# Kernel tuning notes

Hardware: AMD Instinct MI355X
Metric: run time of the kernel (lower is better)

The kernel has to match this reference:

```python
import jax, jax.numpy as jnp
import numpy as np

E = 512        # emb_size
H = 2 * E      # LSTM units
B = 512        # beam/query batch (batched Python-loop states)
K = 32         # padded candidates per state
T = 8          # max_path_length
N_ENT = 50000
N_REL = 5000


def setup_inputs() -> dict:
    key = jax.random.key(0)
    ks = jax.random.split(key, 12)
    f32 = jnp.float32
    ent_emb = jax.random.normal(ks[0], (N_ENT, E), f32) * 0.05
    rel_emb = jax.random.normal(ks[1], (N_REL, E), f32) * 0.05
    relation = jax.random.normal(ks[2], (B, E), f32) * 0.05
    Wx = jax.random.normal(ks[3], (H, 4 * H), f32) * 0.02
    Wh = jax.random.normal(ks[4], (H, 4 * H), f32) * 0.02
    b = jnp.zeros((4 * H,), f32)
    W1 = jax.random.normal(ks[5], (4 * E, 3 * E), f32) * 0.02
    b1 = jnp.zeros((3 * E,), f32)
    W2 = jax.random.normal(ks[6], (3 * E, 2 * E), f32) * 0.02
    b2 = jnp.zeros((2 * E,), f32)
    current_ids = jax.random.randint(ks[7], (T, B), 0, N_ENT)
    prev_rel_ids = jax.random.randint(ks[8], (T, B), 0, N_REL)
    cand_rel_ids = jax.random.randint(ks[9], (T, B, K), 0, N_REL)
    cand_ent_ids = jax.random.randint(ks[10], (T, B, K), 0, N_ENT)
    return {
        "ent_emb": ent_emb, "rel_emb": rel_emb, "relation": relation,
        "Wx": Wx, "Wh": Wh, "b": b,
        "W1": W1, "b1": b1, "W2": W2, "b2": b2,
        "current_ids": current_ids, "prev_rel_ids": prev_rel_ids,
        "cand_rel_ids": cand_rel_ids, "cand_ent_ids": cand_ent_ids,
    }


def reference(ent_emb, rel_emb, relation, Wx, Wh, b, W1, b1, W2, b2,
              current_ids, prev_rel_ids, cand_rel_ids, cand_ent_ids):
    Bh = relation.shape[0]
    units = Wh.shape[0]
    h0 = jnp.zeros((Bh, units), ent_emb.dtype)
    c0 = jnp.zeros((Bh, units), ent_emb.dtype)

    def step(carry, xs):
        h, c = carry
        cur, prl, crel, cent = xs
        # LSTMCell input: concat(prev relation vec, current entity vec)  [B, 2E]
        x = jnp.concatenate([rel_emb[prl], ent_emb[cur]], axis=-1)
        z = x @ Wx + h @ Wh + b                      # [B, 4H], keras gate order i,f,g,o
        i_, f_, g_, o_ = jnp.split(z, 4, axis=-1)
        c = jax.nn.sigmoid(f_) * c + jax.nn.sigmoid(i_) * jnp.tanh(g_)
        h = jax.nn.sigmoid(o_) * jnp.tanh(c)
        # posterior MLP on concat(ent, history, relation)  [B, 4E] -> [B, 2E]
        feat = jax.nn.relu(jnp.concatenate([ent_emb[cur], h, relation], axis=-1) @ W1 + b1)
        feat = jax.nn.relu(feat @ W2 + b2)
        # candidate embeddings: concat(rel vec, to-entity vec)  [B, K, 2E]
        cand = jnp.concatenate([rel_emb[crel], ent_emb[cent]], axis=-1)
        probs = jax.nn.softmax(jnp.einsum('bkd,bd->bk', cand, feat), axis=-1)
        return (h, c), probs

    _, probs = jax.lax.scan(step, (h0, c0),
                            (current_ids, prev_rel_ids, cand_rel_ids, cand_ent_ids))
    return probs  # [T, B, K]
```

## Files before the change

kernel.cpp:

```cpp
#include <hip/hip_runtime.h>
#include <stdint.h>

typedef __attribute__((ext_vector_type(4))) float f32x4;
typedef __attribute__((ext_vector_type(8))) __bf16 bf16x8;
typedef __attribute__((ext_vector_type(8))) unsigned short u16x8;
typedef __attribute__((ext_vector_type(4))) unsigned short u16x4;

typedef const __attribute__((address_space(1))) unsigned int gu32;
typedef __attribute__((address_space(3))) unsigned int lu32;

__device__ __forceinline__ float b2f(unsigned short u) {
  unsigned int x = ((unsigned int)u) << 16;
  float f; __builtin_memcpy(&f, &x, 4); return f;
}
__device__ __forceinline__ unsigned short f2b(float f) {
  unsigned int x; __builtin_memcpy(&x, &f, 4);
  x += 0x7fffu + ((x >> 16) & 1u);
  return (unsigned short)(x >> 16);
}
__device__ __forceinline__ float sigmoidf(float x) {
  return 1.f / (1.f + __expf(-x));
}
__device__ __forceinline__ float tanh_fast(float x) {
  return 1.f - 2.f / (1.f + __expf(2.f * x));
}

__global__ __launch_bounds__(256) void prep1(
    const float* __restrict__ Wx, unsigned short* __restrict__ WxT,
    const float* __restrict__ Wh, unsigned short* __restrict__ WhT,
    const float* __restrict__ W1, unsigned short* __restrict__ W1T,
    const float* __restrict__ W2, unsigned short* __restrict__ W2T,
    const float* __restrict__ ent, const float* __restrict__ rel,
    const float* __restrict__ rln,
    const int* __restrict__ cur, const int* __restrict__ prl,
    unsigned short* __restrict__ Xall, unsigned short* __restrict__ ERall) {
  __shared__ unsigned short tile[64][72];
  const int tid = threadIdx.x;
  int b = blockIdx.x;
  if (b < 3200) {
    const float* in; unsigned short* out; int R, C, bx, by;
    if (b < 1024)      { in = Wx; out = WxT; R = 1024; C = 4096; bx = b & 63; by = b >> 6; }
    else if (b < 2048) { b -= 1024; in = Wh; out = WhT; R = 1024; C = 4096; bx = b & 63; by = b >> 6; }
    else if (b < 2816) { b -= 2048; in = W1; out = W1T; R = 2048; C = 1536; bx = b % 24; by = b / 24; }
    else               { b -= 2816; in = W2; out = W2T; R = 1536; C = 1024; bx = b & 15; by = b >> 4; }
    const int r0 = by * 64, c0 = bx * 64;
    const int r = tid >> 3;
    const int c8 = (tid & 7) * 8;
#pragma unroll
    for (int i = 0; i < 2; i++) {
      const int rr = r + 32*i;
      const float* src = in + (size_t)(r0 + rr) * C + c0 + c8;
      f32x4 a = *(const f32x4*)src;
      f32x4 bb = *(const f32x4*)(src + 4);
      unsigned short tmp[8];
#pragma unroll
      for (int j = 0; j < 4; j++) { tmp[j] = f2b(a[j]); tmp[4+j] = f2b(bb[j]); }
      *(u16x8*)(&tile[rr][c8 ^ (((rr >> 3) & 7) << 3)]) = *(u16x8*)tmp;
    }
    __syncthreads();
    const int rswz = (tid & 7) << 3;
#pragma unroll
    for (int i = 0; i < 2; i++) {
      const int ro = r + 32*i;
      unsigned short tmp[8];
#pragma unroll
      for (int j = 0; j < 8; j++) tmp[j] = tile[c8 + j][ro ^ rswz];
      *(u16x8*)(out + (size_t)(c0 + ro) * R + r0 + c8) = *(u16x8*)tmp;
    }
  } else {
    const int row = b - 3200;
    const int bb = row & 511;
    const int ci = cur[row], ri = prl[row];
    const int half = tid >> 7;
    const int j = tid & 127;
    const float* src;
    if (half == 0) src = (j < 64) ? (rel + (size_t)ri * 512 + j * 8)
                                  : (ent + (size_t)ci * 512 + (j - 64) * 8);
    else           src = (j < 64) ? (ent + (size_t)ci * 512 + j * 8)
                                  : (rln + (size_t)bb * 512 + (j - 64) * 8);
    f32x4 a = *(const f32x4*)src, c = *(const f32x4*)(src + 4);
    unsigned short t[8];
#pragma unroll
    for (int q = 0; q < 4; q++) { t[q] = f2b(a[q]); t[4+q] = f2b(c[q]); }
    unsigned short* dst = (half == 0 ? Xall : ERall) + (size_t)row * 1024 + j * 8;
    *(u16x8*)dst = *(u16x8*)t;
  }
}

__global__ __launch_bounds__(256) void conv_tables(
    const float* __restrict__ ent, unsigned short* __restrict__ entB,
    const float* __restrict__ rel, unsigned short* __restrict__ relB) {
  const long long N0 = 50000LL * 512 / 8, N1 = 5000LL * 512 / 8;
  long long i = (long long)blockIdx.x * 256 + threadIdx.x;
  if (i >= N0 + N1) return;
  const float* in; unsigned short* out;
  if (i < N0) { in = ent; out = entB; }
  else        { in = rel; out = relB; i -= N0; }
  f32x4 a = *(const f32x4*)(in + i * 8);
  f32x4 c = *(const f32x4*)(in + i * 8 + 4);
  unsigned short t[8];
#pragma unroll
  for (int q = 0; q < 4; q++) { t[q] = f2b(a[q]); t[4+q] = f2b(c[q]); }
  *(u16x8*)(out + i * 8) = *(u16x8*)t;
}

template<bool HAS_BIAS, bool DO_RELU, bool PERM_B, bool ASPLIT, bool LSTM0>
__global__ __launch_bounds__(256) void gemm_bf16(
    const unsigned short* __restrict__ A,
    const unsigned short* __restrict__ A2, int lda,
    const unsigned short* __restrict__ BT, int ldb, int K,
    const float* __restrict__ bias,
    unsigned short* __restrict__ Cout, int ldc,
    const float* __restrict__ gbias,
    unsigned short* __restrict__ Hout, float* __restrict__ Cst) {
  __shared__ unsigned short As[128][64];
  __shared__ unsigned short Bs[128][64];
  const int tid = threadIdx.x;
  const int lane = tid & 63;
  const int w = tid >> 6;
  const int wr = w >> 1, wc = w & 1;
  const int m0 = blockIdx.y * 128, n0 = blockIdx.x * 128;
  f32x4 acc[4][4] = {};
  const int srow = lane >> 3;
  const int scol = ((lane & 7) ^ srow) * 8;

  for (int k0 = 0; k0 < K; k0 += 64) {
    const unsigned short* asrc; int ac;
    if (ASPLIT) {
      if (k0 < 512)       { asrc = A;  ac = k0; }
      else if (k0 < 1536) { asrc = A2; ac = k0 - 512; }
      else                { asrc = A;  ac = k0 - 1024; }
    } else { asrc = A; ac = k0; }
#pragma unroll
    for (int i = 0; i < 4; i++) {
      const int c = w * 4 + i;
      const int row = c * 8 + srow;
      __builtin_amdgcn_global_load_lds(
          (gu32*)(asrc + (size_t)(m0 + row) * lda + ac + scol),
          (lu32*)(&As[0][0] + c * 512), 16, 0, 0);
      const int brow = n0 + row;
      const int prow = PERM_B ? (((brow & 3) << 10) + (brow >> 2)) : brow;
      __builtin_amdgcn_global_load_lds(
          (gu32*)(BT + (size_t)prow * ldb + k0 + scol),
          (lu32*)(&Bs[0][0] + c * 512), 16, 0, 0);
    }
    __syncthreads();
#pragma unroll
    for (int ks = 0; ks < 2; ks++) {
      const int kb = ks * 32 + (lane >> 4) * 8;
      const int kswz = kb ^ ((lane & 7) << 3);
      bf16x8 af[4], bfr[4];
#pragma unroll
      for (int m = 0; m < 4; m++)
        af[m] = *reinterpret_cast<const bf16x8*>(&As[wr*64 + m*16 + (lane & 15)][kswz]);
#pragma unroll
      for (int n = 0; n < 4; n++)
        bfr[n] = *reinterpret_cast<const bf16x8*>(&Bs[wc*64 + n*16 + (lane & 15)][kswz]);
#pragma unroll
      for (int m = 0; m < 4; m++)
#pragma unroll
        for (int n = 0; n < 4; n++)
          acc[m][n] = __builtin_amdgcn_mfma_f32_16x16x32_bf16(af[m], bfr[n], acc[m][n], 0, 0, 0);
    }
    __syncthreads();
  }

  const int cn = lane & 15, rb = (lane >> 4) * 4;
  if (LSTM0 && m0 < 512) {
    const int g = lane & 3;
#pragma unroll
    for (int m = 0; m < 4; m++) {
#pragma unroll
      for (int n = 0; n < 4; n++) {
        const int gn = n0 + wc*64 + n*16 + cn;
        const int u = gn >> 2;
        const float gb = gbias[g * 1024 + u];
        const int row0 = m0 + wr*64 + m*16 + rb;
        const float v0 = acc[m][n][0] + gb;
        const float v1 = acc[m][n][1] + gb;
        const float v2 = acc[m][n][2] + gb;
        const float v3 = acc[m][n][3] + gb;
        auto sel = [&](int idx) {
          return idx == 0 ? v0 : idx == 1 ? v1 : idx == 2 ? v2 : v3;
        };
        const float own = sel(g);
        const float r1 = __shfl_xor(sel(g ^ 1), 1);
        const float r2 = __shfl_xor(sel(g ^ 2), 2);
        const float r3 = __shfl_xor(sel(g ^ 3), 3);
        const float zi = g==0 ? own : g==1 ? r1 : g==2 ? r2 : r3;
        const float zg_= g==0 ? r2  : g==1 ? r3 : g==2 ? own: r1;
        const float zo = g==0 ? r3  : g==1 ? r2 : g==2 ? r1 : own;
        const float cnew = sigmoidf(zi) * tanh_fast(zg_);
        const float h = sigmoidf(zo) * tanh_fast(cnew);
        const size_t hidx = (size_t)(row0 + g) * 1024 + u;
        Cst[hidx] = cnew;
        Hout[hidx] = f2b(h);
      }
    }
    return;
  }
#pragma unroll
  for (int m = 0; m < 4; m++) {
#pragma unroll
    for (int n = 0; n < 4; n++) {
      const int gn = n0 + wc*64 + n*16 + cn;
#pragma unroll
      for (int r = 0; r < 4; r++) {
        const int gm = m0 + wr*64 + m*16 + rb + r;
        float v = acc[m][n][r];
        if (HAS_BIAS) v += bias[gn];
        if (DO_RELU)  v = v > 0.f ? v : 0.f;
        Cout[(size_t)gm * ldc + gn] = f2b(v);
      }
    }
  }
}

__global__ __launch_bounds__(512) void zgemm_lstm(
    const unsigned short* __restrict__ A,
    const unsigned short* __restrict__ BT,
    const unsigned short* __restrict__ pre,
    const float* __restrict__ bias,
    unsigned short* __restrict__ Hout,
    float* __restrict__ Cst) {
  __shared__ unsigned short As[2][2][64][64];
  __shared__ unsigned short Bs[2][2][64][64];
  __shared__ f32x4 accL[4][256];
  const int tid = threadIdx.x;
  const int lane = tid & 63;
  const int w = tid >> 6;
  const int q = w >> 2;
  const int wq = w & 3;
  const int wr = wq >> 1, wc = wq & 1;
  const int m0 = blockIdx.y * 64, n0 = blockIdx.x * 64;
  f32x4 acc[2][2] = {};
  const int tq = tid & 255;
  const int srow = lane >> 3;
  const int scol = ((lane & 7) ^ srow) * 8;

  auto STAGE = [&](int buf, int k0) {
    const int kk = q * 512 + k0;
#pragma unroll
    for (int i = 0; i < 2; i++) {
      const int c = wq * 2 + i;
      const int row = c * 8 + srow;
      __builtin_amdgcn_global_load_lds(
          (gu32*)(A + (size_t)(m0 + row) * 1024 + kk + scol),
          (lu32*)(&As[buf][q][0][0] + c * 512), 16, 0, 0);
      const int brow = n0 + row;
      const int prow = ((brow & 3) << 10) + (brow >> 2);
      __builtin_amdgcn_global_load_lds(
          (gu32*)(BT + (size_t)prow * 1024 + kk + scol),
          (lu32*)(&Bs[buf][q][0][0] + c * 512), 16, 0, 0);
    }
  };

  STAGE(0, 0);
  __syncthreads();
  for (int k0 = 0; k0 < 512; k0 += 64) {
    const int buf = (k0 >> 6) & 1;
    if (k0 + 64 < 512) STAGE(buf ^ 1, k0 + 64);
#pragma unroll
    for (int ks = 0; ks < 2; ks++) {
      const int kb = ks * 32 + (lane >> 4) * 8;
      const int kswz = kb ^ ((lane & 7) << 3);
      bf16x8 af[2], bfr[2];
#pragma unroll
      for (int m = 0; m < 2; m++)
        af[m] = *reinterpret_cast<const bf16x8*>(&As[buf][q][wr*32 + m*16 + (lane & 15)][kswz]);
#pragma unroll
      for (int n = 0; n < 2; n++)
        bfr[n] = *reinterpret_cast<const bf16x8*>(&Bs[buf][q][wc*32 + n*16 + (lane & 15)][kswz]);
#pragma unroll
      for (int m = 0; m < 2; m++)
#pragma unroll
        for (int n = 0; n < 2; n++)
          acc[m][n] = __builtin_amdgcn_mfma_f32_16x16x32_bf16(af[m], bfr[n], acc[m][n], 0, 0, 0);
    }
    __syncthreads();
  }

  if (q == 1) {
#pragma unroll
    for (int m = 0; m < 2; m++)
#pragma unroll
      for (int n = 0; n < 2; n++)
        accL[m*2 + n][tq] = acc[m][n];
  }
  __syncthreads();
  if (q == 0) {
    const int cn = lane & 15, rb = (lane >> 4) * 4, g = lane & 3;
#pragma unroll
    for (int m = 0; m < 2; m++) {
#pragma unroll
      for (int n = 0; n < 2; n++) {
        const f32x4 s4 = accL[m*2 + n][tq];
        const int gn = n0 + wc*32 + n*16 + cn;
        const int u = gn >> 2;
        const float gb = bias[g * 1024 + u];
        const int row0 = m0 + wr*32 + m*16 + rb;
        const float v0 = acc[m][n][0] + s4[0] + b2f(pre[(size_t)(row0+0) * 4096 + gn]) + gb;
        const float v1 = acc[m][n][1] + s4[1] + b2f(pre[(size_t)(row0+1) * 4096 + gn]) + gb;
        const float v2 = acc[m][n][2] + s4[2] + b2f(pre[(size_t)(row0+2) * 4096 + gn]) + gb;
        const float v3 = acc[m][n][3] + s4[3] + b2f(pre[(size_t)(row0+3) * 4096 + gn]) + gb;
        auto sel = [&](int idx) {
          return idx == 0 ? v0 : idx == 1 ? v1 : idx == 2 ? v2 : v3;
        };
        const float own = sel(g);
        const float r1 = __shfl_xor(sel(g ^ 1), 1);
        const float r2 = __shfl_xor(sel(g ^ 2), 2);
        const float r3 = __shfl_xor(sel(g ^ 3), 3);
        const float zi = g==0 ? own : g==1 ? r1 : g==2 ? r2 : r3;
        const float zf = g==0 ? r1  : g==1 ? own: g==2 ? r3 : r2;
        const float zg_= g==0 ? r2  : g==1 ? r3 : g==2 ? own: r1;
        const float zo = g==0 ? r3  : g==1 ? r2 : g==2 ? r1 : own;
        const size_t hidx = (size_t)(row0 + g) * 1024 + u;
        const float cnew = sigmoidf(zf) * Cst[hidx] + sigmoidf(zi) * tanh_fast(zg_);
        const float h = sigmoidf(zo) * tanh_fast(cnew);
        Cst[hidx] = cnew;
        Hout[hidx] = f2b(h);
      }
    }
  }
}

__global__ __launch_bounds__(256) void score_softmax(
    const unsigned short* __restrict__ F2,
    const unsigned short* __restrict__ relB,
    const unsigned short* __restrict__ entB,
    const int* __restrict__ crel, const int* __restrict__ cent,
    float* __restrict__ outp) {
  const int b = blockIdx.x;
  const int tid = threadIdx.x;
  const int lane = tid & 63, w = tid >> 6;
  __shared__ float feat[1024];
  __shared__ float logits[32];
  {
    u16x4 fv = ((const u16x4*)(F2 + (size_t)b * 1024))[tid];
#pragma unroll
    for (int j = 0; j < 4; j++) feat[tid * 4 + j] = b2f(fv[j]);
  }
  __syncthreads();
  for (int k = w; k < 32; k += 4) {
    const int ri = crel[b * 32 + k], ei = cent[b * 32 + k];
    u16x8 rv = *(const u16x8*)(relB + (size_t)ri * 512 + lane * 8);
    u16x8 ev = *(const u16x8*)(entB + (size_t)ei * 512 + lane * 8);
    float sum = 0.f;
#pragma unroll
    for (int j = 0; j < 8; j++) {
      sum += b2f(rv[j]) * feat[lane * 8 + j];
      sum += b2f(ev[j]) * feat[512 + lane * 8 + j];
    }
#pragma unroll
    for (int off = 32; off; off >>= 1) sum += __shfl_down(sum, off, 64);
    if (lane == 0) logits[k] = sum;
  }
  __syncthreads();
  if (tid < 32) {
    const float l = logits[tid];
    float mx = l;
#pragma unroll
    for (int off = 16; off; off >>= 1) mx = fmaxf(mx, __shfl_xor(mx, off, 32));
    const float p = __expf(l - mx);
    float s = p;
#pragma unroll
    for (int off = 16; off; off >>= 1) s += __shfl_xor(s, off, 32);
    outp[(size_t)b * 32 + tid] = p / s;
  }
}

extern "C" void kernel_launch(void* const* d_in, const int* in_sizes, int n_in,
                              void* d_out, int out_size, void* d_ws, size_t ws_size,
                              hipStream_t stream) {
  const float* ent      = (const float*)d_in[0];
  const float* rel      = (const float*)d_in[1];
  const float* relation = (const float*)d_in[2];
  const float* Wx       = (const float*)d_in[3];
  const float* Wh       = (const float*)d_in[4];
  const float* bvec     = (const float*)d_in[5];
  const float* W1       = (const float*)d_in[6];
  const float* b1       = (const float*)d_in[7];
  const float* W2       = (const float*)d_in[8];
  const float* b2       = (const float*)d_in[9];
  const int* cur  = (const int*)d_in[10];
  const int* prl  = (const int*)d_in[11];
  const int* crel = (const int*)d_in[12];
  const int* cent = (const int*)d_in[13];
  float* out = (float*)d_out;
  (void)in_sizes; (void)n_in; (void)out_size; (void)ws_size;

  char* wsp = (char*)d_ws;
  auto alloc = [&](size_t bytes) { char* p = wsp; wsp += (bytes + 255) & ~(size_t)255; return p; };
  unsigned short* entB = (unsigned short*)alloc((size_t)50000 * 512 * 2);
  unsigned short* relB = (unsigned short*)alloc((size_t)5000 * 512 * 2);
  unsigned short* WxT  = (unsigned short*)alloc((size_t)4096 * 1024 * 2);
  unsigned short* WhT  = (unsigned short*)alloc((size_t)4096 * 1024 * 2);
  unsigned short* W1T  = (unsigned short*)alloc((size_t)1536 * 2048 * 2);
  unsigned short* W2T  = (unsigned short*)alloc((size_t)1024 * 1536 * 2);
  unsigned short* Xall = (unsigned short*)alloc((size_t)4096 * 1024 * 2);
  unsigned short* ERall= (unsigned short*)alloc((size_t)4096 * 1024 * 2);
  unsigned short* P1   = (unsigned short*)alloc((size_t)4096 * 4096 * 2);
  unsigned short* Hall = (unsigned short*)alloc((size_t)4096 * 1024 * 2);
  unsigned short* F1   = (unsigned short*)alloc((size_t)4096 * 1536 * 2);
  unsigned short* F2   = (unsigned short*)alloc((size_t)4096 * 1024 * 2);
  float*          C    = (float*)         alloc((size_t)512 * 1024 * 4);

  const dim3 blk(256);
  const size_t HS = (size_t)512 * 1024;

  prep1<<<7296, blk, 0, stream>>>(
      Wx, WxT, Wh, WhT, W1, W1T, W2, W2T,
      ent, rel, relation, cur, prl, Xall, ERall);

  gemm_bf16<false,false,true,false,true><<<dim3(32, 32), blk, 0, stream>>>(
      Xall, nullptr, 1024, WxT, 1024, 1024, nullptr, P1, 4096, bvec, Hall, C);

  for (int t = 1; t < 8; t++) {
    zgemm_lstm<<<dim3(64, 8), dim3(512), 0, stream>>>(
        Hall + (size_t)(t - 1) * HS, WhT,
        P1 + (size_t)t * 512 * 4096, bvec,
        Hall + (size_t)t * HS, C);
  }

  gemm_bf16<true,true,false,true,false><<<dim3(12, 32), blk, 0, stream>>>(
      ERall, Hall, 1024, W1T, 2048, 2048, b1, F1, 1536, nullptr, nullptr, nullptr);
  gemm_bf16<true,true,false,false,false><<<dim3(8, 32), blk, 0, stream>>>(
      F1, nullptr, 1536, W2T, 1536, 1536, b2, F2, 1024, nullptr, nullptr, nullptr);

  conv_tables<<<13750, blk, 0, stream>>>(ent, entB, rel, relB);
  score_softmax<<<4096, 256, 0, stream>>>(F2, relB, entB, crel, cent, out);
}
```

Measured before the change: 298.6 us.

## Fold embedding table bf16 conversion into the recurrent LSTM step kernels

```diff
diff --git a/kernel.cpp b/kernel.cpp
--- a/kernel.cpp
+++ b/kernel.cpp
@@ -85,23 +85,6 @@
     unsigned short* dst = (half == 0 ? Xall : ERall) + (size_t)row * 1024 + j * 8;
     *(u16x8*)dst = *(u16x8*)t;
   }
-}
-
-__global__ __launch_bounds__(256) void conv_tables(
-    const float* __restrict__ ent, unsigned short* __restrict__ entB,
-    const float* __restrict__ rel, unsigned short* __restrict__ relB) {
-  const long long N0 = 50000LL * 512 / 8, N1 = 5000LL * 512 / 8;
-  long long i = (long long)blockIdx.x * 256 + threadIdx.x;
-  if (i >= N0 + N1) return;
-  const float* in; unsigned short* out;
-  if (i < N0) { in = ent; out = entB; }
-  else        { in = rel; out = relB; i -= N0; }
-  f32x4 a = *(const f32x4*)(in + i * 8);
-  f32x4 c = *(const f32x4*)(in + i * 8 + 4);
-  unsigned short t[8];
-#pragma unroll
-  for (int q = 0; q < 4; q++) { t[q] = f2b(a[q]); t[4+q] = f2b(c[q]); }
-  *(u16x8*)(out + i * 8) = *(u16x8*)t;
 }
 
 template<bool HAS_BIAS, bool DO_RELU, bool PERM_B, bool ASPLIT, bool LSTM0>
@@ -222,7 +205,10 @@
     const unsigned short* __restrict__ pre,
     const float* __restrict__ bias,
     unsigned short* __restrict__ Hout,
-    float* __restrict__ Cst) {
+    float* __restrict__ Cst,
+    const float* __restrict__ entF, unsigned short* __restrict__ entB,
+    const float* __restrict__ relF, unsigned short* __restrict__ relB,
+    long long conv_base) {
   __shared__ unsigned short As[2][2][64][64];
   __shared__ unsigned short Bs[2][2][64][64];
   __shared__ f32x4 accL[4][256];
@@ -256,6 +242,23 @@
   };
 
   STAGE(0, 0);
+
+  const long long NC0 = 50000LL * 512 / 8;
+  const long long NC  = NC0 + 5000LL * 512 / 8;
+  const long long ci  = conv_base +
+      ((long long)(blockIdx.y * 64 + blockIdx.x) * 512 + tid) * 2;
+  f32x4 cva0, cvb0, cva1, cvb1;
+  const bool cv0 = ci < NC, cv1 = ci + 1 < NC;
+  if (cv0) {
+    const float* p = (ci < NC0) ? entF + ci * 8 : relF + (ci - NC0) * 8;
+    cva0 = *(const f32x4*)p; cvb0 = *(const f32x4*)(p + 4);
+  }
+  if (cv1) {
+    const long long c1 = ci + 1;
+    const float* p = (c1 < NC0) ? entF + c1 * 8 : relF + (c1 - NC0) * 8;
+    cva1 = *(const f32x4*)p; cvb1 = *(const f32x4*)(p + 4);
+  }
+
   __syncthreads();
   for (int k0 = 0; k0 < 512; k0 += 64) {
     const int buf = (k0 >> 6) & 1;
@@ -322,6 +325,22 @@
       }
     }
   }
+
+  if (cv0) {
+    unsigned short* o = (ci < NC0) ? entB + ci * 8 : relB + (ci - NC0) * 8;
+    unsigned short t[8];
+#pragma unroll
+    for (int j = 0; j < 4; j++) { t[j] = f2b(cva0[j]); t[4+j] = f2b(cvb0[j]); }
+    *(u16x8*)o = *(u16x8*)t;
+  }
+  if (cv1) {
+    const long long c1 = ci + 1;
+    unsigned short* o = (c1 < NC0) ? entB + c1 * 8 : relB + (c1 - NC0) * 8;
+    unsigned short t[8];
+#pragma unroll
+    for (int j = 0; j < 4; j++) { t[j] = f2b(cva1[j]); t[4+j] = f2b(cvb1[j]); }
+    *(u16x8*)o = *(u16x8*)t;
+  }
 }
 
 __global__ __launch_bounds__(256) void score_softmax(
@@ -419,7 +438,8 @@
     zgemm_lstm<<<dim3(64, 8), dim3(512), 0, stream>>>(
         Hall + (size_t)(t - 1) * HS, WhT,
         P1 + (size_t)t * 512 * 4096, bvec,
-        Hall + (size_t)t * HS, C);
+        Hall + (size_t)t * HS, C,
+        ent, entB, rel, relB, (long long)(t - 1) * 524288);
   }
 
   gemm_bf16<true,true,false,true,false><<<dim3(12, 32), blk, 0, stream>>>(
@@ -427,6 +447,5 @@
   gemm_bf16<true,true,false,false,false><<<dim3(8, 32), blk, 0, stream>>>(
       F1, nullptr, 1536, W2T, 1536, 1536, b2, F2, 1024, nullptr, nullptr, nullptr);
 
-  conv_tables<<<13750, blk, 0, stream>>>(ent, entB, rel, relB);
   score_softmax<<<4096, 256, 0, stream>>>(F2, relB, entB, crel, cent, out);
 }
```

Result: slower. 306.6 us (+2.7%).
